# Performance work log

Measured on AMD Instinct MI355X. Metric: run time of the kernel, lower is better.

## Reference

```python
import jax, jax.numpy as jnp
import numpy as np

EMB = 768
HEADS = 12
HEAD_DIM = EMB // HEADS
LN_EPS = 1e-5


def _layernorm(x, g, b):
    mu = jnp.mean(x, axis=-1, keepdims=True)
    var = jnp.mean(jnp.square(x - mu), axis=-1, keepdims=True)
    return (x - mu) * jax.lax.rsqrt(var + LN_EPS) * g + b


def _att_block(x, ln_g, ln_b, w_qkv, b_qkv, w_proj, b_proj):
    # x: [b, n, e]
    B, N, E = x.shape
    h, d = HEADS, HEAD_DIM
    qkv = _layernorm(x, ln_g, ln_b) @ w_qkv.T + b_qkv          # [b, n, 3e]
    # einops 'b n (h d qkv)': last axis factors as (h, d, 3), qkv innermost
    qkv = qkv.reshape(B, N, h, d, 3)
    qkv = jnp.moveaxis(qkv, (4, 2), (0, 2))                    # [3, b, h, n, d]
    q, k, v = qkv[0], qkv[1], qkv[2]
    scale = d ** (-0.5)
    # NOTE: original code DIVIDES by scale (= multiplies by sqrt(d)) -- faithful
    scores = jnp.einsum('bhqd,bhkd->bhqk', q, k) / scale       # [b, h, n, n]
    attn = jax.nn.softmax(scores, axis=-1)
    out = jnp.einsum('bhqk,bhkd->bhqd', attn, v)               # [b, h, n, d]
    out = out.transpose(0, 2, 1, 3).reshape(B, N, E)           # [b, n, e]
    return x + out @ w_proj.T + b_proj


def setup_inputs() -> dict:
    key = jax.random.key(0)
    ks = jax.random.split(key, 8)
    B, N, E = 2, 2048, EMB
    s = E ** (-0.5)
    return {
        'modal1': jax.random.normal(ks[0], (B, N, E), jnp.float32),
        'modal2': jax.random.normal(ks[1], (B, N, E), jnp.float32),
        'ln1_g': jnp.ones((E,), jnp.float32),
        'ln1_b': jnp.zeros((E,), jnp.float32),
        'w_qkv1': jax.random.normal(ks[2], (3 * E, E), jnp.float32) * s,
        'b_qkv1': jnp.zeros((3 * E,), jnp.float32),
        'w_proj1': jax.random.normal(ks[3], (E, E), jnp.float32) * s,
        'b_proj1': jnp.zeros((E,), jnp.float32),
        'ln2_g': jnp.ones((E,), jnp.float32),
        'ln2_b': jnp.zeros((E,), jnp.float32),
        'w_qkv2': jax.random.normal(ks[4], (3 * E, E), jnp.float32) * s,
        'b_qkv2': jnp.zeros((3 * E,), jnp.float32),
        'w_proj2': jax.random.normal(ks[5], (E, E), jnp.float32) * s,
        'b_proj2': jnp.zeros((E,), jnp.float32),
    }


def reference(modal1, modal2, ln1_g, ln1_b, w_qkv1, b_qkv1, w_proj1, b_proj1,
              ln2_g, ln2_b, w_qkv2, b_qkv2, w_proj2, b_proj2):
    out1 = _att_block(modal1, ln1_g, ln1_b, w_qkv1, b_qkv1, w_proj1, b_proj1)
    out2 = _att_block(modal2, ln2_g, ln2_b, w_qkv2, b_qkv2, w_proj2, b_proj2)
    return (out1, out2)
```

## Files before the change

kernel.cpp:

```cpp
#include <hip/hip_runtime.h>
#include <hip/hip_bf16.h>


typedef unsigned short u16;
typedef unsigned int   u32;
typedef __attribute__((ext_vector_type(4))) float          floatx4;
typedef __attribute__((ext_vector_type(8))) short          shortx8;

#define EMB   768
#define SEQ   2048
#define NHEAD 12
#define HDIM  64
#define RPM   4096
#define NROW  8192
#define NUNIT 48
#define LDA   40
#define LDK   72

__device__ __forceinline__ float bf2f(u16 h) {
  union { u32 u; float f; } v; v.u = ((u32)h) << 16; return v.f;
}
__device__ __forceinline__ u16 f2bf(float f) {
  union { float f; u32 u; } v; v.f = f;
  u32 r = v.u + 0x7fffu + ((v.u >> 16) & 1u);
  return (u16)(r >> 16);
}
__device__ __forceinline__ u16 f2bf_tr(float f) {
  union { float f; u32 u; } v; v.f = f;
  return (u16)(v.u >> 16);
}
__device__ __forceinline__ float swz_max16(float v) {
  union { float f; int i; } a;
  a.f = v; a.i = __builtin_amdgcn_ds_swizzle(a.i, 0x041F); v = fmaxf(v, a.f);
  a.f = v; a.i = __builtin_amdgcn_ds_swizzle(a.i, 0x081F); v = fmaxf(v, a.f);
  a.f = v; a.i = __builtin_amdgcn_ds_swizzle(a.i, 0x101F); v = fmaxf(v, a.f);
  a.f = v; a.i = __builtin_amdgcn_ds_swizzle(a.i, 0x201F); v = fmaxf(v, a.f);
  return v;
}

__global__ __launch_bounds__(256) void prep_wq(
    const float* __restrict__ wq1, const float* __restrict__ wq2,
    u16* __restrict__ wh, u16* __restrict__ wl)
{
  int bx = blockIdx.x;
  int modal = bx / 2304, rowp = bx % 2304;
  int typ = rowp / 768, hd = rowp % 768;
  const float* W = (modal ? wq2 : wq1) + (size_t)(hd * 3 + typ) * EMB;
  size_t dst = (size_t)bx * EMB;
  int t = threadIdx.x;
  #pragma unroll
  for (int i = 0; i < 3; ++i) {
    int e = t + i * 256;
    float v = W[e];
    u16 h = f2bf(v);
    wh[dst + e] = h;
    wl[dst + e] = f2bf(v - bf2f(h));
  }
}

__global__ __launch_bounds__(256) void prep_wp(
    const float* __restrict__ wp1, const float* __restrict__ wp2,
    u16* __restrict__ wh)
{
  int bx = blockIdx.x;
  int modal = bx / 768, row = bx % 768;
  const float* W = (modal ? wp2 : wp1) + (size_t)row * EMB;
  size_t dst = (size_t)bx * EMB;
  int t = threadIdx.x;
  #pragma unroll
  for (int i = 0; i < 3; ++i) {
    int e = t + i * 256;
    wh[dst + e] = f2bf(W[e]);
  }
}

__global__ __launch_bounds__(256) void k_ln(
    const float* __restrict__ x1, const float* __restrict__ x2,
    const float* __restrict__ g1, const float* __restrict__ b1,
    const float* __restrict__ g2, const float* __restrict__ b2,
    u16* __restrict__ xn_hi, u16* __restrict__ xn_lo)
{
  int row = blockIdx.x;
  int modal = row >> 12;
  const float* x = modal ? x2 : x1;
  const float* g = modal ? g2 : g1;
  const float* bb = modal ? b2 : b1;
  int r = row & (RPM - 1);
  const float* xr = x + (size_t)r * EMB;
  int t = threadIdx.x;
  float v0 = xr[t], v1 = xr[t + 256], v2 = xr[t + 512];
  float s = v0 + v1 + v2;
  float s2 = v0 * v0 + v1 * v1 + v2 * v2;
  #pragma unroll
  for (int m = 1; m < 64; m <<= 1) { s += __shfl_xor(s, m); s2 += __shfl_xor(s2, m); }
  __shared__ float ls[4], ls2[4];
  int w = t >> 6;
  if ((t & 63) == 0) { ls[w] = s; ls2[w] = s2; }
  __syncthreads();
  s = ls[0] + ls[1] + ls[2] + ls[3];
  s2 = ls2[0] + ls2[1] + ls2[2] + ls2[3];
  float mu = s * (1.0f / EMB);
  float var = s2 * (1.0f / EMB) - mu * mu;
  float rs = rsqrtf(var + 1e-5f);
  size_t base = (size_t)row * EMB;
  float vv[3] = { v0, v1, v2 };
  #pragma unroll
  for (int i = 0; i < 3; ++i) {
    int e = t + i * 256;
    float xn = (vv[i] - mu) * rs * g[e] + bb[e];
    u16 h = f2bf(xn);
    xn_hi[base + e] = h;
    xn_lo[base + e] = f2bf(xn - bf2f(h));
  }
}

__global__ __launch_bounds__(256) void k_qkv(
    const u16* __restrict__ xn_hi, const u16* __restrict__ xn_lo,
    const u16* __restrict__ wqh, const u16* __restrict__ wql,
    const float* __restrict__ bq1, const float* __restrict__ bq2,
    u16* __restrict__ q_hi, u16* __restrict__ q_lo,
    u16* __restrict__ k_hi, u16* __restrict__ k_lo,
    u16* __restrict__ vT)
{
  int mt = blockIdx.x, ntile = blockIdx.y, modal = blockIdx.z;
  const float* BQ = modal ? bq2 : bq1;
  int typ = ntile / 6;
  int hd0 = (ntile % 6) * 128;

  __shared__ u16 As_hi[128 * LDA], As_lo[128 * LDA], Wh[128 * LDA], Wl[128 * LDA];

  int tid = threadIdx.x, lane = tid & 63, w = tid >> 6;
  int wm = (w >> 1) * 64, wn = (w & 1) * 64;
  int lc = lane & 15, lq = lane >> 4;

  floatx4 acc[4][4] = {};
  size_t arow0 = (size_t)(modal * RPM + mt * 128) * EMB;
  size_t wrow0 = (size_t)(modal * 2304 + typ * 768 + hd0) * EMB;

  for (int k0 = 0; k0 < EMB; k0 += 32) {
    #pragma unroll
    for (int i = 0; i < 2; ++i) {
      int c = tid + i * 256;
      int rr = c >> 2, cc = (c & 3) * 8;
      size_t go = (size_t)rr * EMB + k0 + cc;
      *(shortx8*)&As_hi[rr * LDA + cc] = *(const shortx8*)(xn_hi + arow0 + go);
      *(shortx8*)&Wh[rr * LDA + cc]    = *(const shortx8*)(wqh + wrow0 + go);
      if (typ != 2) {
        *(shortx8*)&As_lo[rr * LDA + cc] = *(const shortx8*)(xn_lo + arow0 + go);
        *(shortx8*)&Wl[rr * LDA + cc]    = *(const shortx8*)(wql + wrow0 + go);
      }
    }
    __syncthreads();
    shortx8 ah[4], al[4], wh[4], wl[4];
    #pragma unroll
    for (int i = 0; i < 4; ++i) {
      ah[i] = *(const shortx8*)&As_hi[(wm + i * 16 + lc) * LDA + lq * 8];
      wh[i] = *(const shortx8*)&Wh[(wn + i * 16 + lc) * LDA + lq * 8];
      if (typ != 2) {
        al[i] = *(const shortx8*)&As_lo[(wm + i * 16 + lc) * LDA + lq * 8];
        wl[i] = *(const shortx8*)&Wl[(wn + i * 16 + lc) * LDA + lq * 8];
      }
    }
    #pragma unroll
    for (int i = 0; i < 4; ++i)
      #pragma unroll
      for (int jn = 0; jn < 4; ++jn) {
        acc[i][jn] = __builtin_amdgcn_mfma_f32_16x16x32_bf16(ah[i], wh[jn], acc[i][jn], 0, 0, 0);
        if (typ != 2) {
          acc[i][jn] = __builtin_amdgcn_mfma_f32_16x16x32_bf16(al[i], wh[jn], acc[i][jn], 0, 0, 0);
          acc[i][jn] = __builtin_amdgcn_mfma_f32_16x16x32_bf16(ah[i], wl[jn], acc[i][jn], 0, 0, 0);
        }
      }
    __syncthreads();
  }

  #pragma unroll
  for (int i = 0; i < 4; ++i) {
    int mrow0 = mt * 128 + wm + i * 16 + lq * 4;
    #pragma unroll
    for (int jn = 0; jn < 4; ++jn) {
      int colp = hd0 + wn + jn * 16 + lc;
      int h = colp >> 6, d = colp & 63;
      float bias = BQ[colp * 3 + typ];
      #pragma unroll
      for (int r = 0; r < 4; ++r) {
        int mrow = mrow0 + r;
        int b = mrow >> 11, nq = mrow & (SEQ - 1);
        int uu = modal * 24 + b * 12 + h;
        float val = acc[i][jn][r] + bias;
        if (typ == 0) {
          size_t o = ((size_t)uu * SEQ + nq) * HDIM + d;
          u16 hh = f2bf(val); q_hi[o] = hh; q_lo[o] = f2bf(val - bf2f(hh));
        } else if (typ == 1) {
          size_t o = ((size_t)uu * SEQ + nq) * HDIM + d;
          u16 hh = f2bf(val); k_hi[o] = hh; k_lo[o] = f2bf(val - bf2f(hh));
        } else {
          vT[((size_t)uu * HDIM + d) * SEQ + nq] = f2bf(val);
        }
      }
    }
  }
}

__global__ __launch_bounds__(256) void k_attn(
    const u16* __restrict__ q_hi, const u16* __restrict__ q_lo,
    const u16* __restrict__ k_hi, const u16* __restrict__ k_lo,
    const u16* __restrict__ vT, u16* __restrict__ attn_out)
{
  int qt = blockIdx.x, u = blockIdx.y;
  __shared__ u16 Kh[64 * LDK], Kl[64 * LDK], Vs[64 * LDK];
  __shared__ u16 Ps[4][32 * LDK];

  int tid = threadIdx.x, lane = tid & 63, w = tid >> 6;
  int lc = lane & 15, lq = lane >> 4;
  u16* psw = &Ps[w][0];

  shortx8 qh[2][2], ql[2][2];
  #pragma unroll
  for (int mi = 0; mi < 2; ++mi) {
    size_t qb = ((size_t)u * SEQ + qt * 128 + w * 32 + mi * 16 + lc) * HDIM + lq * 8;
    qh[mi][0] = *(const shortx8*)(q_hi + qb);
    qh[mi][1] = *(const shortx8*)(q_hi + qb + 32);
    ql[mi][0] = *(const shortx8*)(q_lo + qb);
    ql[mi][1] = *(const shortx8*)(q_lo + qb + 32);
  }

  shortx8 ONES;
  #pragma unroll
  for (int j = 0; j < 8; ++j) ONES[j] = (short)0x3F80;

  floatx4 O[2][4] = {};
  floatx4 Osum[2] = {};
  float mrow[2][4];
  #pragma unroll
  for (int mi = 0; mi < 2; ++mi)
    #pragma unroll
    for (int r = 0; r < 4; ++r) mrow[mi][r] = -1e30f;
  const float Cs = 11.5415603271f;

  int c0 = tid, c1 = tid + 256;
  int r0 = c0 >> 3, cc0 = (c0 & 7) * 8;
  int r1 = c1 >> 3, cc1 = (c1 & 7) * 8;
  const u16* khp0 = k_hi + ((size_t)u * SEQ + r0) * HDIM + cc0;
  const u16* khp1 = k_hi + ((size_t)u * SEQ + r1) * HDIM + cc1;
  const u16* klp0 = k_lo + ((size_t)u * SEQ + r0) * HDIM + cc0;
  const u16* klp1 = k_lo + ((size_t)u * SEQ + r1) * HDIM + cc1;
  const u16* vp0  = vT + ((size_t)u * HDIM + r0) * SEQ + cc0;
  const u16* vp1  = vT + ((size_t)u * HDIM + r1) * SEQ + cc1;

  for (int kc = 0; kc < SEQ; kc += 64) {
    *(shortx8*)&Kh[r0 * LDK + cc0] = *(const shortx8*)(khp0 + (size_t)kc * HDIM);
    *(shortx8*)&Kh[r1 * LDK + cc1] = *(const shortx8*)(khp1 + (size_t)kc * HDIM);
    *(shortx8*)&Kl[r0 * LDK + cc0] = *(const shortx8*)(klp0 + (size_t)kc * HDIM);
    *(shortx8*)&Kl[r1 * LDK + cc1] = *(const shortx8*)(klp1 + (size_t)kc * HDIM);
    *(shortx8*)&Vs[r0 * LDK + cc0] = *(const shortx8*)(vp0 + kc);
    *(shortx8*)&Vs[r1 * LDK + cc1] = *(const shortx8*)(vp1 + kc);
    __syncthreads();

    floatx4 S[2][4] = {};
    #pragma unroll
    for (int nt = 0; nt < 4; ++nt)
      #pragma unroll
      for (int ks = 0; ks < 2; ++ks) {
        shortx8 kf = *(const shortx8*)&Kh[(nt * 16 + lc) * LDK + ks * 32 + lq * 8];
        shortx8 lf = *(const shortx8*)&Kl[(nt * 16 + lc) * LDK + ks * 32 + lq * 8];
        #pragma unroll
        for (int mi = 0; mi < 2; ++mi) {
          S[mi][nt] = __builtin_amdgcn_mfma_f32_16x16x32_bf16(qh[mi][ks], kf, S[mi][nt], 0, 0, 0);
          S[mi][nt] = __builtin_amdgcn_mfma_f32_16x16x32_bf16(ql[mi][ks], kf, S[mi][nt], 0, 0, 0);
          S[mi][nt] = __builtin_amdgcn_mfma_f32_16x16x32_bf16(qh[mi][ks], lf, S[mi][nt], 0, 0, 0);
        }
      }
    #pragma unroll
    for (int mi = 0; mi < 2; ++mi)
      #pragma unroll
      for (int nt = 0; nt < 4; ++nt) S[mi][nt] *= Cs;

    #pragma unroll
    for (int mi = 0; mi < 2; ++mi) {
      float alpha[4];
      #pragma unroll
      for (int r = 0; r < 4; ++r) {
        float mc = fmaxf(fmaxf(S[mi][0][r], S[mi][1][r]), fmaxf(S[mi][2][r], S[mi][3][r]));
        mc = swz_max16(mc);
        float mn = fmaxf(mrow[mi][r], mc);
        alpha[r] = __builtin_amdgcn_exp2f(mrow[mi][r] - mn);
        mrow[mi][r] = mn;
      }
      #pragma unroll
      for (int nt = 0; nt < 4; ++nt)
        #pragma unroll
        for (int r = 0; r < 4; ++r) {
          float e = __builtin_amdgcn_exp2f(S[mi][nt][r] - mrow[mi][r]);
          psw[(mi * 16 + lq * 4 + r) * LDK + nt * 16 + lc] = f2bf_tr(e);
        }
      #pragma unroll
      for (int nt = 0; nt < 4; ++nt)
        #pragma unroll
        for (int r = 0; r < 4; ++r) O[mi][nt][r] *= alpha[r];
      #pragma unroll
      for (int r = 0; r < 4; ++r) Osum[mi][r] *= alpha[r];
    }

    #pragma unroll
    for (int ks = 0; ks < 2; ++ks) {
      shortx8 pf[2];
      #pragma unroll
      for (int mi = 0; mi < 2; ++mi)
        pf[mi] = *(const shortx8*)&psw[(mi * 16 + lc) * LDK + ks * 32 + lq * 8];
      #pragma unroll
      for (int nt = 0; nt < 4; ++nt) {
        shortx8 vf = *(const shortx8*)&Vs[(nt * 16 + lc) * LDK + ks * 32 + lq * 8];
        #pragma unroll
        for (int mi = 0; mi < 2; ++mi)
          O[mi][nt] = __builtin_amdgcn_mfma_f32_16x16x32_bf16(pf[mi], vf, O[mi][nt], 0, 0, 0);
      }
      #pragma unroll
      for (int mi = 0; mi < 2; ++mi)
        Osum[mi] = __builtin_amdgcn_mfma_f32_16x16x32_bf16(pf[mi], ONES, Osum[mi], 0, 0, 0);
    }
    __syncthreads();
  }

  int modal = u / 24, b = (u / 12) & 1, h = u % 12;
  #pragma unroll
  for (int mi = 0; mi < 2; ++mi)
    #pragma unroll
    for (int r = 0; r < 4; ++r) {
      float rl = __builtin_amdgcn_rcpf(Osum[mi][r]);
      int qrow = qt * 128 + w * 32 + mi * 16 + lq * 4 + r;
      size_t ob = ((size_t)(modal * RPM + b * SEQ + qrow)) * EMB + h * 64 + lc;
      #pragma unroll
      for (int nt = 0; nt < 4; ++nt)
        attn_out[ob + nt * 16] = f2bf(O[mi][nt][r] * rl);
    }
}

__global__ __launch_bounds__(256) void k_proj(
    const u16* __restrict__ ao, const u16* __restrict__ wph,
    const float* __restrict__ x1, const float* __restrict__ x2,
    const float* __restrict__ bp1, const float* __restrict__ bp2,
    float* __restrict__ out)
{
  int mt = blockIdx.x, ntile = blockIdx.y, modal = blockIdx.z;
  const float* BP = modal ? bp2 : bp1;
  const float* x  = modal ? x2 : x1;

  __shared__ u16 As[128 * LDA], Ws[128 * LDA];
  int tid = threadIdx.x, lane = tid & 63, w = tid >> 6;
  int wm = (w >> 1) * 64, wn = (w & 1) * 64;
  int lc = lane & 15, lq = lane >> 4;

  floatx4 acc[4][4] = {};
  size_t arow0 = (size_t)(modal * RPM + mt * 128) * EMB;
  int col0 = ntile * 128;
  size_t wrow0 = (size_t)(modal * 768 + col0) * EMB;

  for (int k0 = 0; k0 < EMB; k0 += 32) {
    #pragma unroll
    for (int i = 0; i < 2; ++i) {
      int c = tid + i * 256;
      int rr = c >> 2, cc = (c & 3) * 8;
      size_t go = (size_t)rr * EMB + k0 + cc;
      *(shortx8*)&As[rr * LDA + cc] = *(const shortx8*)(ao + arow0 + go);
      *(shortx8*)&Ws[rr * LDA + cc] = *(const shortx8*)(wph + wrow0 + go);
    }
    __syncthreads();
    shortx8 af[4], wf[4];
    #pragma unroll
    for (int i = 0; i < 4; ++i) {
      af[i] = *(const shortx8*)&As[(wm + i * 16 + lc) * LDA + lq * 8];
      wf[i] = *(const shortx8*)&Ws[(wn + i * 16 + lc) * LDA + lq * 8];
    }
    #pragma unroll
    for (int i = 0; i < 4; ++i)
      #pragma unroll
      for (int jn = 0; jn < 4; ++jn)
        acc[i][jn] = __builtin_amdgcn_mfma_f32_16x16x32_bf16(af[i], wf[jn], acc[i][jn], 0, 0, 0);
    __syncthreads();
  }

  #pragma unroll
  for (int i = 0; i < 4; ++i) {
    int mrow0 = mt * 128 + wm + i * 16 + lq * 4;
    #pragma unroll
    for (int jn = 0; jn < 4; ++jn) {
      int col = col0 + wn + jn * 16 + lc;
      float bias = BP[col];
      #pragma unroll
      for (int r = 0; r < 4; ++r) {
        int mrow = mrow0 + r;
        float val = acc[i][jn][r] + bias + x[(size_t)mrow * EMB + col];
        out[((size_t)(modal * RPM + mrow)) * EMB + col] = val;
      }
    }
  }
}

extern "C" void kernel_launch(void* const* d_in, const int* in_sizes, int n_in,
                              void* d_out, int out_size, void* d_ws, size_t ws_size,
                              hipStream_t stream) {
  const float* modal1 = (const float*)d_in[0];
  const float* modal2 = (const float*)d_in[1];
  const float* ln1_g  = (const float*)d_in[2];
  const float* ln1_b  = (const float*)d_in[3];
  const float* w_qkv1 = (const float*)d_in[4];
  const float* b_qkv1 = (const float*)d_in[5];
  const float* w_proj1= (const float*)d_in[6];
  const float* b_proj1= (const float*)d_in[7];
  const float* ln2_g  = (const float*)d_in[8];
  const float* ln2_b  = (const float*)d_in[9];
  const float* w_qkv2 = (const float*)d_in[10];
  const float* b_qkv2 = (const float*)d_in[11];
  const float* w_proj2= (const float*)d_in[12];
  const float* b_proj2= (const float*)d_in[13];
  float* out = (float*)d_out;

  const size_t BUFE = (size_t)NROW * EMB;
  const size_t WQE  = (size_t)2 * 2304 * EMB;
  u16* xn_hi = (u16*)d_ws;
  u16* xn_lo = xn_hi + BUFE;
  u16* q_hi  = xn_lo + BUFE;
  u16* q_lo  = q_hi + BUFE;
  u16* k_hi  = q_lo + BUFE;
  u16* k_lo  = k_hi + BUFE;
  u16* vT    = k_lo + BUFE;
  u16* wq_h  = vT + BUFE;
  u16* wq_l  = wq_h + WQE;
  u16* attn  = xn_hi;
  u16* wp_h  = q_lo;

  prep_wq<<<4608, 256, 0, stream>>>(w_qkv1, w_qkv2, wq_h, wq_l);
  k_ln<<<NROW, 256, 0, stream>>>(modal1, modal2, ln1_g, ln1_b, ln2_g, ln2_b, xn_hi, xn_lo);
  dim3 g2(32, 18, 2);
  k_qkv<<<g2, 256, 0, stream>>>(xn_hi, xn_lo, wq_h, wq_l, b_qkv1, b_qkv2,
                                q_hi, q_lo, k_hi, k_lo, vT);
  dim3 g3(16, 48);
  k_attn<<<g3, 256, 0, stream>>>(q_hi, q_lo, k_hi, k_lo, vT, attn);
  prep_wp<<<1536, 256, 0, stream>>>(w_proj1, w_proj2, wp_h);
  dim3 g4(32, 6, 2);
  k_proj<<<g4, 256, 0, stream>>>(attn, wp_h, modal1, modal2, b_proj1, b_proj2, out);
}
```

Baseline: 407.3 us.

## Register-prefetch next K tiles in GEMM and attention loops; fold softmax scale

Adds register double-buffering to the QKV GEMM, attention and projection kernels: the global loads for the next K-slice are issued right after the barrier, so their latency overlaps the MFMA work on the current tile. The attention grid is transposed so head units vary fastest. The separate multiply of the score tile by the softmax scale is folded into the max and into an fma inside exp2. The cost is more live registers, which could lower occupancy.

```diff
diff --git a/kernel.cpp b/kernel.cpp
--- a/kernel.cpp
+++ b/kernel.cpp
@@ -137,20 +137,39 @@
   size_t arow0 = (size_t)(modal * RPM + mt * 128) * EMB;
   size_t wrow0 = (size_t)(modal * 2304 + typ * 768 + hd0) * EMB;
 
+  int c0 = tid, c1 = tid + 256;
+  int r0 = c0 >> 2, cc0 = (c0 & 3) * 8;
+  int r1 = c1 >> 2, cc1 = (c1 & 3) * 8;
+  size_t go0 = (size_t)r0 * EMB + cc0, go1 = (size_t)r1 * EMB + cc1;
+
+  shortx8 pAh0, pAh1, pW0, pW1, pAl0, pAl1, pL0, pL1;
+  #define QKV_LOAD(k0) do { \
+    pAh0 = *(const shortx8*)(xn_hi + arow0 + go0 + (k0)); \
+    pAh1 = *(const shortx8*)(xn_hi + arow0 + go1 + (k0)); \
+    pW0  = *(const shortx8*)(wqh + wrow0 + go0 + (k0)); \
+    pW1  = *(const shortx8*)(wqh + wrow0 + go1 + (k0)); \
+    if (typ != 2) { \
+      pAl0 = *(const shortx8*)(xn_lo + arow0 + go0 + (k0)); \
+      pAl1 = *(const shortx8*)(xn_lo + arow0 + go1 + (k0)); \
+      pL0  = *(const shortx8*)(wql + wrow0 + go0 + (k0)); \
+      pL1  = *(const shortx8*)(wql + wrow0 + go1 + (k0)); \
+    } } while (0)
+
+  QKV_LOAD(0);
   for (int k0 = 0; k0 < EMB; k0 += 32) {
-    #pragma unroll
-    for (int i = 0; i < 2; ++i) {
-      int c = tid + i * 256;
-      int rr = c >> 2, cc = (c & 3) * 8;
-      size_t go = (size_t)rr * EMB + k0 + cc;
-      *(shortx8*)&As_hi[rr * LDA + cc] = *(const shortx8*)(xn_hi + arow0 + go);
-      *(shortx8*)&Wh[rr * LDA + cc]    = *(const shortx8*)(wqh + wrow0 + go);
-      if (typ != 2) {
-        *(shortx8*)&As_lo[rr * LDA + cc] = *(const shortx8*)(xn_lo + arow0 + go);
-        *(shortx8*)&Wl[rr * LDA + cc]    = *(const shortx8*)(wql + wrow0 + go);
-      }
-    }
-    __syncthreads();
+    *(shortx8*)&As_hi[r0 * LDA + cc0] = pAh0;
+    *(shortx8*)&As_hi[r1 * LDA + cc1] = pAh1;
+    *(shortx8*)&Wh[r0 * LDA + cc0]    = pW0;
+    *(shortx8*)&Wh[r1 * LDA + cc1]    = pW1;
+    if (typ != 2) {
+      *(shortx8*)&As_lo[r0 * LDA + cc0] = pAl0;
+      *(shortx8*)&As_lo[r1 * LDA + cc1] = pAl1;
+      *(shortx8*)&Wl[r0 * LDA + cc0]    = pL0;
+      *(shortx8*)&Wl[r1 * LDA + cc1]    = pL1;
+    }
+    __syncthreads();
+    if (k0 + 32 < EMB) QKV_LOAD(k0 + 32);
+
     shortx8 ah[4], al[4], wh[4], wl[4];
     #pragma unroll
     for (int i = 0; i < 4; ++i) {
@@ -173,6 +192,7 @@
       }
     __syncthreads();
   }
+  #undef QKV_LOAD
 
   #pragma unroll
   for (int i = 0; i < 4; ++i) {
@@ -207,7 +227,7 @@
     const u16* __restrict__ k_hi, const u16* __restrict__ k_lo,
     const u16* __restrict__ vT, u16* __restrict__ attn_out)
 {
-  int qt = blockIdx.x, u = blockIdx.y;
+  int u = blockIdx.x, qt = blockIdx.y;
   __shared__ u16 Kh[64 * LDK], Kl[64 * LDK], Vs[64 * LDK];
   __shared__ u16 Ps[4][32 * LDK];
 
@@ -248,14 +268,25 @@
   const u16* vp0  = vT + ((size_t)u * HDIM + r0) * SEQ + cc0;
   const u16* vp1  = vT + ((size_t)u * HDIM + r1) * SEQ + cc1;
 
+  shortx8 p0, p1, p2, p3, p4, p5;
+  #define ATT_LOAD(kc) do { \
+    p0 = *(const shortx8*)(khp0 + (size_t)(kc) * HDIM); \
+    p1 = *(const shortx8*)(khp1 + (size_t)(kc) * HDIM); \
+    p2 = *(const shortx8*)(klp0 + (size_t)(kc) * HDIM); \
+    p3 = *(const shortx8*)(klp1 + (size_t)(kc) * HDIM); \
+    p4 = *(const shortx8*)(vp0 + (kc)); \
+    p5 = *(const shortx8*)(vp1 + (kc)); } while (0)
+
+  ATT_LOAD(0);
   for (int kc = 0; kc < SEQ; kc += 64) {
-    *(shortx8*)&Kh[r0 * LDK + cc0] = *(const shortx8*)(khp0 + (size_t)kc * HDIM);
-    *(shortx8*)&Kh[r1 * LDK + cc1] = *(const shortx8*)(khp1 + (size_t)kc * HDIM);
-    *(shortx8*)&Kl[r0 * LDK + cc0] = *(const shortx8*)(klp0 + (size_t)kc * HDIM);
-    *(shortx8*)&Kl[r1 * LDK + cc1] = *(const shortx8*)(klp1 + (size_t)kc * HDIM);
-    *(shortx8*)&Vs[r0 * LDK + cc0] = *(const shortx8*)(vp0 + kc);
-    *(shortx8*)&Vs[r1 * LDK + cc1] = *(const shortx8*)(vp1 + kc);
-    __syncthreads();
+    *(shortx8*)&Kh[r0 * LDK + cc0] = p0;
+    *(shortx8*)&Kh[r1 * LDK + cc1] = p1;
+    *(shortx8*)&Kl[r0 * LDK + cc0] = p2;
+    *(shortx8*)&Kl[r1 * LDK + cc1] = p3;
+    *(shortx8*)&Vs[r0 * LDK + cc0] = p4;
+    *(shortx8*)&Vs[r1 * LDK + cc1] = p5;
+    __syncthreads();
+    if (kc + 64 < SEQ) ATT_LOAD(kc + 64);
 
     floatx4 S[2][4] = {};
     #pragma unroll
@@ -271,10 +302,6 @@
           S[mi][nt] = __builtin_amdgcn_mfma_f32_16x16x32_bf16(qh[mi][ks], lf, S[mi][nt], 0, 0, 0);
         }
       }
-    #pragma unroll
-    for (int mi = 0; mi < 2; ++mi)
-      #pragma unroll
-      for (int nt = 0; nt < 4; ++nt) S[mi][nt] *= Cs;
 
     #pragma unroll
     for (int mi = 0; mi < 2; ++mi) {
@@ -283,7 +310,7 @@
       for (int r = 0; r < 4; ++r) {
         float mc = fmaxf(fmaxf(S[mi][0][r], S[mi][1][r]), fmaxf(S[mi][2][r], S[mi][3][r]));
         mc = swz_max16(mc);
-        float mn = fmaxf(mrow[mi][r], mc);
+        float mn = fmaxf(mrow[mi][r], mc * Cs);
         alpha[r] = __builtin_amdgcn_exp2f(mrow[mi][r] - mn);
         mrow[mi][r] = mn;
       }
@@ -291,7 +318,7 @@
       for (int nt = 0; nt < 4; ++nt)
         #pragma unroll
         for (int r = 0; r < 4; ++r) {
-          float e = __builtin_amdgcn_exp2f(S[mi][nt][r] - mrow[mi][r]);
+          float e = __builtin_amdgcn_exp2f(fmaf(S[mi][nt][r], Cs, -mrow[mi][r]));
           psw[(mi * 16 + lq * 4 + r) * LDK + nt * 16 + lc] = f2bf_tr(e);
         }
       #pragma unroll
@@ -321,6 +348,7 @@
     }
     __syncthreads();
   }
+  #undef ATT_LOAD
 
   int modal = u / 24, b = (u / 12) & 1, h = u % 12;
   #pragma unroll
@@ -356,16 +384,27 @@
   int col0 = ntile * 128;
   size_t wrow0 = (size_t)(modal * 768 + col0) * EMB;
 
+  int c0 = tid, c1 = tid + 256;
+  int r0 = c0 >> 2, cc0 = (c0 & 3) * 8;
+  int r1 = c1 >> 2, cc1 = (c1 & 3) * 8;
+  size_t go0 = (size_t)r0 * EMB + cc0, go1 = (size_t)r1 * EMB + cc1;
+
+  shortx8 pA0, pA1, pW0, pW1;
+  #define PROJ_LOAD(k0) do { \
+    pA0 = *(const shortx8*)(ao + arow0 + go0 + (k0)); \
+    pA1 = *(const shortx8*)(ao + arow0 + go1 + (k0)); \
+    pW0 = *(const shortx8*)(wph + wrow0 + go0 + (k0)); \
+    pW1 = *(const shortx8*)(wph + wrow0 + go1 + (k0)); } while (0)
+
+  PROJ_LOAD(0);
   for (int k0 = 0; k0 < EMB; k0 += 32) {
-    #pragma unroll
-    for (int i = 0; i < 2; ++i) {
-      int c = tid + i * 256;
-      int rr = c >> 2, cc = (c & 3) * 8;
-      size_t go = (size_t)rr * EMB + k0 + cc;
-      *(shortx8*)&As[rr * LDA + cc] = *(const shortx8*)(ao + arow0 + go);
-      *(shortx8*)&Ws[rr * LDA + cc] = *(const shortx8*)(wph + wrow0 + go);
-    }
-    __syncthreads();
+    *(shortx8*)&As[r0 * LDA + cc0] = pA0;
+    *(shortx8*)&As[r1 * LDA + cc1] = pA1;
+    *(shortx8*)&Ws[r0 * LDA + cc0] = pW0;
+    *(shortx8*)&Ws[r1 * LDA + cc1] = pW1;
+    __syncthreads();
+    if (k0 + 32 < EMB) PROJ_LOAD(k0 + 32);
+
     shortx8 af[4], wf[4];
     #pragma unroll
     for (int i = 0; i < 4; ++i) {
@@ -379,6 +418,7 @@
         acc[i][jn] = __builtin_amdgcn_mfma_f32_16x16x32_bf16(af[i], wf[jn], acc[i][jn], 0, 0, 0);
     __syncthreads();
   }
+  #undef PROJ_LOAD
 
   #pragma unroll
   for (int i = 0; i < 4; ++i) {
@@ -435,7 +475,7 @@
   dim3 g2(32, 18, 2);
   k_qkv<<<g2, 256, 0, stream>>>(xn_hi, xn_lo, wq_h, wq_l, b_qkv1, b_qkv2,
                                 q_hi, q_lo, k_hi, k_lo, vT);
-  dim3 g3(16, 48);
+  dim3 g3(48, 16);
   k_attn<<<g3, 256, 0, stream>>>(q_hi, q_lo, k_hi, k_lo, vT, attn);
   prep_wp<<<1536, 256, 0, stream>>>(w_proj1, w_proj2, wp_h);
   dim3 g4(32, 6, 2);
```

After: 428.8 us. 5.3% more time.

## Use async global-to-LDS loads with XOR swizzle and double-buffer attention K/V

Applied to the files above, without the earlier changes.

Replaces the register-staged global-to-shared copies in the QKV, attention and projection kernels with direct global_load_lds 16-byte transfers. The padded shared layouts become unpadded tiles addressed through an XOR swizzle so that the fragment reads avoid bank conflicts. The attention kernel double-buffers its K/V tiles so the next chunk is fetched while the current one is computed, and it folds the score scale into the exp2 through an fma. The attention grid is also transposed, which changes the order in which blocks are scheduled. The risk is in correctness: the async copies rely on the global_load_lds lane-to-LDS mapping and on the prefetch being waited for before the next iteration reads it, and nothing explicit such as a vmcnt wait is added.

```diff
diff --git a/kernel.cpp b/kernel.cpp
--- a/kernel.cpp
+++ b/kernel.cpp
@@ -14,8 +14,6 @@
 #define RPM   4096
 #define NROW  8192
 #define NUNIT 48
-#define LDA   40
-#define LDK   72
 
 __device__ __forceinline__ float bf2f(u16 h) {
   union { u32 u; float f; } v; v.u = ((u32)h) << 16; return v.f;
@@ -37,6 +35,15 @@
   a.f = v; a.i = __builtin_amdgcn_ds_swizzle(a.i, 0x201F); v = fmaxf(v, a.f);
   return v;
 }
+
+__device__ __forceinline__ void async16(const u16* g, u16* l) {
+  __builtin_amdgcn_global_load_lds(
+      (const __attribute__((address_space(1))) u32*)g,
+      (__attribute__((address_space(3))) u32*)l, 16, 0, 0);
+}
+
+#define SWZ8(row, lg) (((row) << 6) + ((((lg) ^ ((row) & 7))) << 3))
+#define SWZ4(row, lg) (((row) << 5) + ((((lg) ^ ((row) & 3))) << 3))
 
 __global__ __launch_bounds__(256) void prep_wq(
     const float* __restrict__ wq1, const float* __restrict__ wq2,
@@ -127,7 +134,7 @@
   int typ = ntile / 6;
   int hd0 = (ntile % 6) * 128;
 
-  __shared__ u16 As_hi[128 * LDA], As_lo[128 * LDA], Wh[128 * LDA], Wl[128 * LDA];
+  __shared__ u16 Ah[128 * 32], Al[128 * 32], Bh[128 * 32], Bl[128 * 32];
 
   int tid = threadIdx.x, lane = tid & 63, w = tid >> 6;
   int wm = (w >> 1) * 64, wn = (w & 1) * 64;
@@ -137,28 +144,40 @@
   size_t arow0 = (size_t)(modal * RPM + mt * 128) * EMB;
   size_t wrow0 = (size_t)(modal * 2304 + typ * 768 + hd0) * EMB;
 
+  int rsub = lane >> 2;
+  int g4 = (lane & 3) ^ (rsub & 3);
+  const u16 *sA[2], *sAl[2], *sW[2], *sWl[2];
+  int ldst[2];
+  #pragma unroll
+  for (int seg = 0; seg < 2; ++seg) {
+    int row = w * 32 + seg * 16 + rsub;
+    sA[seg]  = xn_hi + arow0 + (size_t)row * EMB + g4 * 8;
+    sAl[seg] = xn_lo + arow0 + (size_t)row * EMB + g4 * 8;
+    sW[seg]  = wqh + wrow0 + (size_t)row * EMB + g4 * 8;
+    sWl[seg] = wql + wrow0 + (size_t)row * EMB + g4 * 8;
+    ldst[seg] = (w * 32 + seg * 16) * 32;
+  }
+
   for (int k0 = 0; k0 < EMB; k0 += 32) {
     #pragma unroll
-    for (int i = 0; i < 2; ++i) {
-      int c = tid + i * 256;
-      int rr = c >> 2, cc = (c & 3) * 8;
-      size_t go = (size_t)rr * EMB + k0 + cc;
-      *(shortx8*)&As_hi[rr * LDA + cc] = *(const shortx8*)(xn_hi + arow0 + go);
-      *(shortx8*)&Wh[rr * LDA + cc]    = *(const shortx8*)(wqh + wrow0 + go);
+    for (int seg = 0; seg < 2; ++seg) {
+      async16(sA[seg] + k0, &Ah[ldst[seg]]);
+      async16(sW[seg] + k0, &Bh[ldst[seg]]);
       if (typ != 2) {
-        *(shortx8*)&As_lo[rr * LDA + cc] = *(const shortx8*)(xn_lo + arow0 + go);
-        *(shortx8*)&Wl[rr * LDA + cc]    = *(const shortx8*)(wql + wrow0 + go);
+        async16(sAl[seg] + k0, &Al[ldst[seg]]);
+        async16(sWl[seg] + k0, &Bl[ldst[seg]]);
       }
     }
     __syncthreads();
+
     shortx8 ah[4], al[4], wh[4], wl[4];
     #pragma unroll
     for (int i = 0; i < 4; ++i) {
-      ah[i] = *(const shortx8*)&As_hi[(wm + i * 16 + lc) * LDA + lq * 8];
-      wh[i] = *(const shortx8*)&Wh[(wn + i * 16 + lc) * LDA + lq * 8];
+      ah[i] = *(const shortx8*)&Ah[SWZ4(wm + i * 16 + lc, lq)];
+      wh[i] = *(const shortx8*)&Bh[SWZ4(wn + i * 16 + lc, lq)];
       if (typ != 2) {
-        al[i] = *(const shortx8*)&As_lo[(wm + i * 16 + lc) * LDA + lq * 8];
-        wl[i] = *(const shortx8*)&Wl[(wn + i * 16 + lc) * LDA + lq * 8];
+        al[i] = *(const shortx8*)&Al[SWZ4(wm + i * 16 + lc, lq)];
+        wl[i] = *(const shortx8*)&Bl[SWZ4(wn + i * 16 + lc, lq)];
       }
     }
     #pragma unroll
@@ -207,9 +226,9 @@
     const u16* __restrict__ k_hi, const u16* __restrict__ k_lo,
     const u16* __restrict__ vT, u16* __restrict__ attn_out)
 {
-  int qt = blockIdx.x, u = blockIdx.y;
-  __shared__ u16 Kh[64 * LDK], Kl[64 * LDK], Vs[64 * LDK];
-  __shared__ u16 Ps[4][32 * LDK];
+  int u = blockIdx.x, qt = blockIdx.y;
+  __shared__ u16 KV[2][3][64 * 64];
+  __shared__ u16 Ps[4][32 * 64];
 
   int tid = threadIdx.x, lane = tid & 63, w = tid >> 6;
   int lc = lane & 15, lq = lane >> 4;
@@ -238,32 +257,46 @@
     for (int r = 0; r < 4; ++r) mrow[mi][r] = -1e30f;
   const float Cs = 11.5415603271f;
 
-  int c0 = tid, c1 = tid + 256;
-  int r0 = c0 >> 3, cc0 = (c0 & 7) * 8;
-  int r1 = c1 >> 3, cc1 = (c1 & 7) * 8;
-  const u16* khp0 = k_hi + ((size_t)u * SEQ + r0) * HDIM + cc0;
-  const u16* khp1 = k_hi + ((size_t)u * SEQ + r1) * HDIM + cc1;
-  const u16* klp0 = k_lo + ((size_t)u * SEQ + r0) * HDIM + cc0;
-  const u16* klp1 = k_lo + ((size_t)u * SEQ + r1) * HDIM + cc1;
-  const u16* vp0  = vT + ((size_t)u * HDIM + r0) * SEQ + cc0;
-  const u16* vp1  = vT + ((size_t)u * HDIM + r1) * SEQ + cc1;
+  int rsub = lane >> 3;
+  int g8 = (lane & 7) ^ rsub;
+  const u16 *sKh[2], *sKl[2], *sV[2];
+  int ldst[2];
+  #pragma unroll
+  for (int seg = 0; seg < 2; ++seg) {
+    int row = w * 16 + seg * 8 + rsub;
+    sKh[seg] = k_hi + ((size_t)u * SEQ + row) * HDIM + g8 * 8;
+    sKl[seg] = k_lo + ((size_t)u * SEQ + row) * HDIM + g8 * 8;
+    sV[seg]  = vT + ((size_t)u * HDIM + row) * SEQ + g8 * 8;
+    ldst[seg] = (w * 16 + seg * 8) * 64;
+  }
+
+  #pragma unroll
+  for (int seg = 0; seg < 2; ++seg) {
+    async16(sKh[seg], &KV[0][0][ldst[seg]]);
+    async16(sKl[seg], &KV[0][1][ldst[seg]]);
+    async16(sV[seg],  &KV[0][2][ldst[seg]]);
+  }
+  __syncthreads();
 
   for (int kc = 0; kc < SEQ; kc += 64) {
-    *(shortx8*)&Kh[r0 * LDK + cc0] = *(const shortx8*)(khp0 + (size_t)kc * HDIM);
-    *(shortx8*)&Kh[r1 * LDK + cc1] = *(const shortx8*)(khp1 + (size_t)kc * HDIM);
-    *(shortx8*)&Kl[r0 * LDK + cc0] = *(const shortx8*)(klp0 + (size_t)kc * HDIM);
-    *(shortx8*)&Kl[r1 * LDK + cc1] = *(const shortx8*)(klp1 + (size_t)kc * HDIM);
-    *(shortx8*)&Vs[r0 * LDK + cc0] = *(const shortx8*)(vp0 + kc);
-    *(shortx8*)&Vs[r1 * LDK + cc1] = *(const shortx8*)(vp1 + kc);
-    __syncthreads();
+    int b = (kc >> 6) & 1;
+    if (kc + 64 < SEQ) {
+      int nb = b ^ 1;
+      #pragma unroll
+      for (int seg = 0; seg < 2; ++seg) {
+        async16(sKh[seg] + (size_t)(kc + 64) * HDIM, &KV[nb][0][ldst[seg]]);
+        async16(sKl[seg] + (size_t)(kc + 64) * HDIM, &KV[nb][1][ldst[seg]]);
+        async16(sV[seg] + (kc + 64),                 &KV[nb][2][ldst[seg]]);
+      }
+    }
 
     floatx4 S[2][4] = {};
     #pragma unroll
     for (int nt = 0; nt < 4; ++nt)
       #pragma unroll
       for (int ks = 0; ks < 2; ++ks) {
-        shortx8 kf = *(const shortx8*)&Kh[(nt * 16 + lc) * LDK + ks * 32 + lq * 8];
-        shortx8 lf = *(const shortx8*)&Kl[(nt * 16 + lc) * LDK + ks * 32 + lq * 8];
+        shortx8 kf = *(const shortx8*)&KV[b][0][SWZ8(nt * 16 + lc, ks * 4 + lq)];
+        shortx8 lf = *(const shortx8*)&KV[b][1][SWZ8(nt * 16 + lc, ks * 4 + lq)];
         #pragma unroll
         for (int mi = 0; mi < 2; ++mi) {
           S[mi][nt] = __builtin_amdgcn_mfma_f32_16x16x32_bf16(qh[mi][ks], kf, S[mi][nt], 0, 0, 0);
@@ -271,10 +304,6 @@
           S[mi][nt] = __builtin_amdgcn_mfma_f32_16x16x32_bf16(qh[mi][ks], lf, S[mi][nt], 0, 0, 0);
         }
       }
-    #pragma unroll
-    for (int mi = 0; mi < 2; ++mi)
-      #pragma unroll
-      for (int nt = 0; nt < 4; ++nt) S[mi][nt] *= Cs;
 
     #pragma unroll
     for (int mi = 0; mi < 2; ++mi) {
@@ -283,7 +312,7 @@
       for (int r = 0; r < 4; ++r) {
         float mc = fmaxf(fmaxf(S[mi][0][r], S[mi][1][r]), fmaxf(S[mi][2][r], S[mi][3][r]));
         mc = swz_max16(mc);
-        float mn = fmaxf(mrow[mi][r], mc);
+        float mn = fmaxf(mrow[mi][r], mc * Cs);
         alpha[r] = __builtin_amdgcn_exp2f(mrow[mi][r] - mn);
         mrow[mi][r] = mn;
       }
@@ -291,8 +320,10 @@
       for (int nt = 0; nt < 4; ++nt)
         #pragma unroll
         for (int r = 0; r < 4; ++r) {
-          float e = __builtin_amdgcn_exp2f(S[mi][nt][r] - mrow[mi][r]);
-          psw[(mi * 16 + lq * 4 + r) * LDK + nt * 16 + lc] = f2bf_tr(e);
+          float e = __builtin_amdgcn_exp2f(fmaf(S[mi][nt][r], Cs, -mrow[mi][r]));
+          int prow = mi * 16 + lq * 4 + r;
+          int pcol = nt * 16 + lc;
+          psw[(prow << 6) + ((((pcol >> 3) ^ (prow & 7))) << 3) + (pcol & 7)] = f2bf_tr(e);
         }
       #pragma unroll
       for (int nt = 0; nt < 4; ++nt)
@@ -307,10 +338,10 @@
       shortx8 pf[2];
       #pragma unroll
       for (int mi = 0; mi < 2; ++mi)
-        pf[mi] = *(const shortx8*)&psw[(mi * 16 + lc) * LDK + ks * 32 + lq * 8];
+        pf[mi] = *(const shortx8*)&psw[SWZ8(mi * 16 + lc, ks * 4 + lq)];
       #pragma unroll
       for (int nt = 0; nt < 4; ++nt) {
-        shortx8 vf = *(const shortx8*)&Vs[(nt * 16 + lc) * LDK + ks * 32 + lq * 8];
+        shortx8 vf = *(const shortx8*)&KV[b][2][SWZ8(nt * 16 + lc, ks * 4 + lq)];
         #pragma unroll
         for (int mi = 0; mi < 2; ++mi)
           O[mi][nt] = __builtin_amdgcn_mfma_f32_16x16x32_bf16(pf[mi], vf, O[mi][nt], 0, 0, 0);
@@ -322,14 +353,14 @@
     __syncthreads();
   }
 
-  int modal = u / 24, b = (u / 12) & 1, h = u % 12;
+  int modal = u / 24, b2 = (u / 12) & 1, h = u % 12;
   #pragma unroll
   for (int mi = 0; mi < 2; ++mi)
     #pragma unroll
     for (int r = 0; r < 4; ++r) {
       float rl = __builtin_amdgcn_rcpf(Osum[mi][r]);
       int qrow = qt * 128 + w * 32 + mi * 16 + lq * 4 + r;
-      size_t ob = ((size_t)(modal * RPM + b * SEQ + qrow)) * EMB + h * 64 + lc;
+      size_t ob = ((size_t)(modal * RPM + b2 * SEQ + qrow)) * EMB + h * 64 + lc;
       #pragma unroll
       for (int nt = 0; nt < 4; ++nt)
         attn_out[ob + nt * 16] = f2bf(O[mi][nt][r] * rl);
@@ -346,7 +377,7 @@
   const float* BP = modal ? bp2 : bp1;
   const float* x  = modal ? x2 : x1;
 
-  __shared__ u16 As[128 * LDA], Ws[128 * LDA];
+  __shared__ u16 As[128 * 32], Ws[128 * 32];
   int tid = threadIdx.x, lane = tid & 63, w = tid >> 6;
   int wm = (w >> 1) * 64, wn = (w & 1) * 64;
   int lc = lane & 15, lq = lane >> 4;
@@ -356,21 +387,31 @@
   int col0 = ntile * 128;
   size_t wrow0 = (size_t)(modal * 768 + col0) * EMB;
 
+  int rsub = lane >> 2;
+  int g4 = (lane & 3) ^ (rsub & 3);
+  const u16 *sA[2], *sW[2];
+  int ldst[2];
+  #pragma unroll
+  for (int seg = 0; seg < 2; ++seg) {
+    int row = w * 32 + seg * 16 + rsub;
+    sA[seg] = ao + arow0 + (size_t)row * EMB + g4 * 8;
+    sW[seg] = wph + wrow0 + (size_t)row * EMB + g4 * 8;
+    ldst[seg] = (w * 32 + seg * 16) * 32;
+  }
+
   for (int k0 = 0; k0 < EMB; k0 += 32) {
     #pragma unroll
-    for (int i = 0; i < 2; ++i) {
-      int c = tid + i * 256;
-      int rr = c >> 2, cc = (c & 3) * 8;
-      size_t go = (size_t)rr * EMB + k0 + cc;
-      *(shortx8*)&As[rr * LDA + cc] = *(const shortx8*)(ao + arow0 + go);
-      *(shortx8*)&Ws[rr * LDA + cc] = *(const shortx8*)(wph + wrow0 + go);
+    for (int seg = 0; seg < 2; ++seg) {
+      async16(sA[seg] + k0, &As[ldst[seg]]);
+      async16(sW[seg] + k0, &Ws[ldst[seg]]);
     }
     __syncthreads();
+
     shortx8 af[4], wf[4];
     #pragma unroll
     for (int i = 0; i < 4; ++i) {
-      af[i] = *(const shortx8*)&As[(wm + i * 16 + lc) * LDA + lq * 8];
-      wf[i] = *(const shortx8*)&Ws[(wn + i * 16 + lc) * LDA + lq * 8];
+      af[i] = *(const shortx8*)&As[SWZ4(wm + i * 16 + lc, lq)];
+      wf[i] = *(const shortx8*)&Ws[SWZ4(wn + i * 16 + lc, lq)];
     }
     #pragma unroll
     for (int i = 0; i < 4; ++i)
@@ -435,7 +476,7 @@
   dim3 g2(32, 18, 2);
   k_qkv<<<g2, 256, 0, stream>>>(xn_hi, xn_lo, wq_h, wq_l, b_qkv1, b_qkv2,
                                 q_hi, q_lo, k_hi, k_lo, vT);
-  dim3 g3(16, 48);
+  dim3 g3(48, 16);
   k_attn<<<g3, 256, 0, stream>>>(q_hi, q_lo, k_hi, k_lo, vT, attn);
   prep_wp<<<1536, 256, 0, stream>>>(w_proj1, w_proj2, wp_h);
   dim3 g4(32, 6, 2);
```

Result: slower. 426.9 us (+4.8%).
